# Optimization experiments

Measured on AMD Instinct MI355X. Metric: run time of the kernel, lower is better.

The kernel has to match this reference:

```python
import jax, jax.numpy as jnp
import numpy as np

B = 32          # batch
IH = IW = 32    # image_size
N = IH * IW     # tokens = 1024
INP = 256
OUP = 256
H = 8           # heads
D = 32          # dim_head
INNER = H * D   # 256
TABLE = (2 * IH - 1) * (2 * IW - 1)  # 3969


def _rel_index():
    # exact replica of the torch buffer construction
    coords = np.stack(np.meshgrid(np.arange(IH), np.arange(IW), indexing='ij')).reshape(2, -1)
    rel = coords[:, :, None] - coords[:, None, :]
    rel[0] += IH - 1
    rel[1] += IW - 1
    rel[0] *= 2 * IW - 1
    return (rel[0] + rel[1]).reshape(-1)  # [N*N]


def setup_inputs() -> dict:
    key = jax.random.key(0)
    k0, k1, k2, k3 = jax.random.split(key, 4)
    x = jax.random.normal(k0, (B, N, INP), jnp.float32)
    W_qkv = jax.random.normal(k1, (INP, 3 * INNER), jnp.float32) * 0.02
    bias_table = jax.random.normal(k2, (TABLE, H), jnp.float32) * 0.02
    W_out = jax.random.normal(k3, (INNER, OUP), jnp.float32) * 0.02
    b_out = jnp.zeros((OUP,), jnp.float32)
    rel_index = jnp.asarray(_rel_index(), jnp.int32)
    return {"x": x, "W_qkv": W_qkv, "bias_table": bias_table,
            "W_out": W_out, "b_out": b_out, "rel_index": rel_index}


def reference(x, W_qkv, bias_table, W_out, b_out, rel_index):
    scale = D ** -0.5
    qkv = x @ W_qkv                                   # [B, N, 3*INNER]
    q, k, v = jnp.split(qkv, 3, axis=-1)
    to_heads = lambda t: t.reshape(B, N, H, D).transpose(0, 2, 1, 3)  # b h n d
    q, k, v = to_heads(q), to_heads(k), to_heads(v)
    dots = jnp.einsum('bhid,bhjd->bhij', q, k) * scale  # [B, H, N, N]
    # gather per-head relative position bias: [N*N, H] -> [1, H, N, N]
    bias = bias_table[rel_index].reshape(N, N, H).transpose(2, 0, 1)[None]
    attn = jax.nn.softmax(dots + bias, axis=-1)
    out = jnp.einsum('bhij,bhjd->bhid', attn, v)        # [B, H, N, D]
    out = out.transpose(0, 2, 1, 3).reshape(B, N, INNER)
    return out @ W_out + b_out
```

## Files before the change

kernel.cpp:

```cpp
#include <hip/hip_runtime.h>

typedef __attribute__((ext_vector_type(4))) int            vi4;
typedef __attribute__((ext_vector_type(4))) float          vf4;
typedef __attribute__((ext_vector_type(8))) short          vs8;
typedef __attribute__((ext_vector_type(2))) unsigned int   vu2;
typedef unsigned short u16;
typedef unsigned int   u32;

#define LOG2E  1.4426950408889634f
#define QSCALE 0.2550484109f

static __device__ __forceinline__ u16 f2bf(float f) {
  u32 u = __builtin_bit_cast(u32, f);
  u32 r = (u + 0x7fffu + ((u >> 16) & 1u)) >> 16;
  return (u16)r;
}
static __device__ __forceinline__ float bfu_lo(u32 u) {
  return __builtin_bit_cast(float, u << 16);
}
static __device__ __forceinline__ float bfu_hi(u32 u) {
  return __builtin_bit_cast(float, u & 0xffff0000u);
}
static __device__ __forceinline__ u32 packbf_perm(float a, float b) {
  return __builtin_amdgcn_perm(__builtin_bit_cast(u32, b),
                               __builtin_bit_cast(u32, a), 0x07060302u);
}
static __device__ __forceinline__ vf4 unpack_bias(const u32* grp, int tj) {
  u32 b0 = grp[tj * 2], b1 = grp[tj * 2 + 1];
  vf4 c; c[0] = bfu_lo(b0); c[1] = bfu_hi(b0);
  c[2] = bfu_lo(b1); c[3] = bfu_hi(b1);
  return c;
}

static __device__ __forceinline__ void ldsdma16(void* lds, const void* g) {
  __builtin_amdgcn_global_load_lds(
      (const u32 __attribute__((address_space(1)))*)g,
      (u32 __attribute__((address_space(3)))*)lds, 16, 0, 0);
}

__global__ void prep_all(const float* __restrict__ x, u16* __restrict__ xbf,
                         const float* __restrict__ Wqkv, u16* __restrict__ WqkvT,
                         const float* __restrict__ Wout, u16* __restrict__ WoutT,
                         const int* __restrict__ rel, const float* __restrict__ table,
                         u32* __restrict__ bias_pk, float* __restrict__ bias_f,
                         int use_f32) {
  __shared__ __align__(8) u16 relS[64 * 32];
  int bid = blockIdx.x, tid = threadIdx.x;
  if (bid < 8192) {
    int i = (bid * 256 + tid) * 4;
    vf4 v = *(const vf4*)&x[i];
    u32 lo = (u32)f2bf(v[0]) | ((u32)f2bf(v[1]) << 16);
    u32 hi = (u32)f2bf(v[2]) | ((u32)f2bf(v[3]) << 16);
    vu2 o; o[0] = lo; o[1] = hi;
    *(vu2*)&xbf[i] = o;
  } else if (bid < 9216) {
    const float* src; u16* dst; int C, idx;
    if (bid < 8960) { src = Wqkv; dst = WqkvT; C = 768; idx = (bid - 8192) * 256 + tid; }
    else            { src = Wout; dst = WoutT; C = 256; idx = (bid - 8960) * 256 + tid; }
    int r = idx / C, c = idx - r * C;
    dst[c * 256 + r] = f2bf(src[idx]);
  } else {
    int b2 = bid - 9216;
    int qt = b2 >> 6, t = (b2 >> 2) & 15, s = b2 & 3;
    int ti = s >> 1, jhalf = s & 1;
    int wave = tid >> 6, quad = (tid >> 4) & 3, l15 = tid & 15;
    int jbase = t * 64 + jhalf * 32;

#pragma unroll
    for (int p = 0; p < 2; ++p) {
      int task = p * 256 + tid;
      int q = task >> 3, unit = task & 7;
      int m = qt * 128 + (q >> 4) * 32 + ti * 16 + (q & 15);
      vi4 v = *(const vi4*)&rel[m * 1024 + jbase + unit * 4];
      vu2 pk;
      pk[0] = (u32)(v[0] & 0xffff) | ((u32)v[1] << 16);
      pk[1] = (u32)(v[2] & 0xffff) | ((u32)v[3] << 16);
      *(vu2*)&relS[q * 32 + unit * 4] = pk;
    }
    __syncthreads();

    int mrow = wave * 16 + l15;
    float vals[8][8];
#pragma unroll
    for (int tjl = 0; tjl < 2; ++tjl)
#pragma unroll
      for (int r = 0; r < 4; ++r) {
        int idx = relS[mrow * 32 + tjl * 16 + quad * 4 + r];
        vf4 a = *(const vf4*)&table[idx * 8];
        vf4 bb = *(const vf4*)&table[idx * 8 + 4];
#pragma unroll
        for (int h = 0; h < 4; ++h) {
          vals[tjl * 4 + r][h] = a[h];
          vals[tjl * 4 + r][h + 4] = bb[h];
        }
      }
    if (use_f32) {
#pragma unroll
      for (int h = 0; h < 8; ++h)
#pragma unroll
        for (int tjl = 0; tjl < 2; ++tjl) {
          int frag = ti * 4 + jhalf * 2 + tjl;
          vf4 v;
#pragma unroll
          for (int r = 0; r < 4; ++r) v[r] = vals[tjl * 4 + r][h] * LOG2E;
          *(vf4*)&bias_f[(((h * 8 + qt) * 16 + t) * 8 + frag) * 1024 + tid * 4] = v;
        }
    } else {
#pragma unroll
      for (int h = 0; h < 8; ++h) {
        u32 o[4];
#pragma unroll
        for (int tjl = 0; tjl < 2; ++tjl)
#pragma unroll
          for (int p = 0; p < 2; ++p) {
            u32 lo = f2bf(vals[tjl * 4 + 2 * p][h] * LOG2E);
            u32 hi = f2bf(vals[tjl * 4 + 2 * p + 1][h] * LOG2E);
            o[tjl * 2 + p] = lo | (hi << 16);
          }
        *(vi4*)&bias_pk[h * 524288 + (qt * 16 + t) * 4096 + tid * 16 + s * 4] =
            *(const vi4*)o;
      }
    }
  }
}

template <int EPI>
__global__ __launch_bounds__(256, 2) void gemm_k256(
    const u16* __restrict__ A, const u16* __restrict__ Bt,
    u16* __restrict__ q_out, u16* __restrict__ k_out, u16* __restrict__ v_out,
    float* __restrict__ c_out, const float* __restrict__ bias) {
  __shared__ __align__(16) u16 SMEM[EPI == 0 ? 128 * 136 : 8192];
  u16* As = SMEM;
  u16* Bs = SMEM + 4096;
  const int tid = threadIdx.x;
  const int lane15 = tid & 15, quad = (tid >> 4) & 3, wave = tid >> 6;
  const int wr = (wave & 1) * 64, wc = (wave >> 1) * 64;
  const int m0 = blockIdx.y * 128, n0 = blockIdx.x * 128;

  const u16* Ag = &A[(m0 + (tid >> 2)) * 256 + (tid & 3) * 8];
  const u16* Bg = &Bt[(n0 + (tid >> 2)) * 256 + (tid & 3) * 8];
  u16* AsW = &As[wave * 512];
  u16* BsW = &Bs[wave * 512];

  const vf4 z4 = {0.f, 0.f, 0.f, 0.f};
  vf4 acc[4][4];
#pragma unroll
  for (int i = 0; i < 4; ++i)
#pragma unroll
    for (int j = 0; j < 4; ++j) acc[i][j] = z4;

  for (int k0 = 0; k0 < 256; k0 += 32) {
    __syncthreads();
    ldsdma16(AsW,        Ag + k0);
    ldsdma16(AsW + 2048, Ag + k0 + 64 * 256);
    ldsdma16(BsW,        Bg + k0);
    ldsdma16(BsW + 2048, Bg + k0 + 64 * 256);
    __syncthreads();
    vs8 af[4], bfr[4];
#pragma unroll
    for (int ti = 0; ti < 4; ++ti)
      af[ti] = *(const vs8*)&As[(wr + ti * 16 + lane15) * 32 + quad * 8];
#pragma unroll
    for (int tj = 0; tj < 4; ++tj)
      bfr[tj] = *(const vs8*)&Bs[(wc + tj * 16 + lane15) * 32 + quad * 8];
#pragma unroll
    for (int ti = 0; ti < 4; ++ti)
#pragma unroll
      for (int tj = 0; tj < 4; ++tj)
        acc[ti][tj] = __builtin_amdgcn_mfma_f32_16x16x32_bf16(af[ti], bfr[tj],
                                                              acc[ti][tj], 0, 0, 0);
  }

  if (EPI == 0) {
    const int which = n0 >> 8;
    const int bb = m0 >> 10, nn0 = m0 & 1023;
    u16* Cs = SMEM;
    __syncthreads();
    if (which < 2) {
      float sc = (which == 0) ? QSCALE : 1.f;
#pragma unroll
      for (int tj = 0; tj < 4; ++tj) {
        int col = wc + tj * 16 + lane15;
#pragma unroll
        for (int ti = 0; ti < 4; ++ti) {
          int row0 = wr + ti * 16 + quad * 4;
#pragma unroll
          for (int r = 0; r < 4; ++r)
            Cs[(row0 + r) * 136 + col] = f2bf(acc[ti][tj][r] * sc);
        }
      }
      __syncthreads();
      u16* base = (which == 0) ? q_out : k_out;
#pragma unroll
      for (int hp = 0; hp < 4; ++hp) {
        int hh = ((n0 + hp * 32) >> 5) & 7;
        u16* pb = base + ((bb * 8 + hh) * 1024 + nn0) * 32;
#pragma unroll
        for (int p2 = 0; p2 < 2; ++p2) {
          int task = p2 * 256 + tid;
          int row = task >> 2, unit = task & 3;
          vi4 v = *(const vi4*)&Cs[row * 136 + hp * 32 + unit * 8];
          *(vi4*)&pb[row * 32 + unit * 8] = v;
        }
      }
    } else {
#pragma unroll
      for (int tj = 0; tj < 4; ++tj) {
        int col = wc + tj * 16 + lane15;
#pragma unroll
        for (int ti = 0; ti < 4; ++ti) {
          int row0 = wr + ti * 16 + quad * 4;
          vu2 pk;
          pk[0] = (u32)f2bf(acc[ti][tj][0]) | ((u32)f2bf(acc[ti][tj][1]) << 16);
          pk[1] = (u32)f2bf(acc[ti][tj][2]) | ((u32)f2bf(acc[ti][tj][3]) << 16);
          *(vu2*)&Cs[col * 136 + row0] = pk;
        }
      }
      __syncthreads();
#pragma unroll
      for (int p = 0; p < 8; ++p) {
        int task = p * 256 + tid;
        int col = task >> 4, unit = task & 15;
        int cg = n0 + col;
        int hh = (cg >> 5) & 7, d = cg & 31;
        vi4 v = *(const vi4*)&Cs[col * 136 + unit * 8];
        *(vi4*)&v_out[((bb * 8 + hh) * 32 + d) * 1024 + nn0 + unit * 8] = v;
      }
    }
  } else {
#pragma unroll
    for (int tj = 0; tj < 4; ++tj) {
      int colg = n0 + wc + tj * 16 + lane15;
      float bo = bias[colg];
#pragma unroll
      for (int ti = 0; ti < 4; ++ti)
#pragma unroll
        for (int r = 0; r < 4; ++r) {
          int rowg = m0 + wr + ti * 16 + quad * 4 + r;
          c_out[rowg * 256 + colg] = acc[ti][tj][r] + bo;
        }
    }
  }
}

template <int BF32>
__global__ __launch_bounds__(256, 4) void flash_attn(
    const u16* __restrict__ Qws, const u16* __restrict__ Kws,
    const u16* __restrict__ Vtws, const void* __restrict__ biasv,
    u16* __restrict__ Ows) {
  __shared__ __align__(16) u16 Ks[2][64 * 40];
  __shared__ __align__(16) u16 Vt[2][32 * 72];
  __shared__ __align__(16) u16 Ps[4][32 * 72];

  const int tid = threadIdx.x;
  const int l15 = tid & 15, quad = (tid >> 4) & 3, wave = tid >> 6;
  const int bid = blockIdx.x;
  const int h = bid & 7, b = (bid >> 3) & 31, qt = bid >> 8;
  const int q0 = qt * 128;
  const int bh = b * 8 + h;
  const u16* Qbase = Qws + (bh * 1024 + q0) * 32;
  const u16* Kbase = Kws + bh * 1024 * 32;
  const u16* Vbase = Vtws + bh * 32 * 1024;
  const float* Bf = (const float*)biasv + (h * 8 + qt) * 131072 + tid * 4;
  const u32*  Bpk = (const u32*)biasv + h * 524288 + qt * 65536 + tid * 16;

  const int kv_j = tid >> 2, kv_seg = (tid & 3) * 8;
  const int v_d = tid >> 3,  v_seg = (tid & 7) * 8;
  const u16* Kg = Kbase + kv_j * 32 + kv_seg;
  const u16* Vg = Vbase + v_d * 1024 + v_seg;

  vs8 af[2];
#pragma unroll
  for (int ti = 0; ti < 2; ++ti)
    af[ti] = *(const vs8*)&Qbase[(wave * 32 + ti * 16 + l15) * 32 + quad * 8];

  vi4 kreg = *(const vi4*)Kg;
  vi4 vreg = *(const vi4*)Vg;
  *(vi4*)&Ks[0][kv_j * 40 + kv_seg] = kreg;
  *(vi4*)&Vt[0][v_d * 72 + v_seg] = vreg;

  vf4 b0pre[4];
  vi4 bpk_pre[2];
  if (BF32) {
#pragma unroll
    for (int i = 0; i < 4; ++i) b0pre[i] = *(const vf4*)&Bf[i * 1024];
  } else {
#pragma unroll
    for (int i = 0; i < 2; ++i) bpk_pre[i] = *(const vi4*)(Bpk + i * 4);
  }

  const vf4 z4 = {0.f, 0.f, 0.f, 0.f};
  vf4 O[2][2];
  O[0][0] = z4; O[0][1] = z4; O[1][0] = z4; O[1][1] = z4;
  vf4 Lacc[2];
  Lacc[0] = z4; Lacc[1] = z4;

  vs8 onesv;
#pragma unroll
  for (int i = 0; i < 8; ++i) onesv[i] = (short)0x3F80;

  u16* PwBase = Ps[wave];

  for (int t = 0; t < 16; ++t) {
    const int cur = t & 1, nxt = cur ^ 1;
    __syncthreads();

    if (t < 15) {
      kreg = *(const vi4*)(Kg + (t + 1) * 2048);
      vreg = *(const vi4*)(Vg + (t + 1) * 64);
    }
    vf4 b1cur[4], b0nxt[4];
    vi4 bpk1[2], bpk_n[2];
    if (BF32) {
#pragma unroll
      for (int i = 0; i < 4; ++i)
        b1cur[i] = *(const vf4*)&Bf[(t * 8 + 4 + i) * 1024];
      if (t < 15) {
#pragma unroll
        for (int i = 0; i < 4; ++i)
          b0nxt[i] = *(const vf4*)&Bf[((t + 1) * 8 + i) * 1024];
      }
    } else {
      bpk1[0] = *(const vi4*)(Bpk + t * 4096 + 8);
      bpk1[1] = *(const vi4*)(Bpk + t * 4096 + 12);
      if (t < 15) {
        bpk_n[0] = *(const vi4*)(Bpk + (t + 1) * 4096);
        bpk_n[1] = *(const vi4*)(Bpk + (t + 1) * 4096 + 4);
      }
    }

    vs8 bk[4];
#pragma unroll
    for (int tj = 0; tj < 4; ++tj)
      bk[tj] = *(const vs8*)&Ks[cur][(tj * 16 + l15) * 40 + quad * 8];

#pragma unroll
    for (int tj = 0; tj < 4; ++tj) {
      vf4 c = BF32 ? b0pre[tj] : unpack_bias((const u32*)bpk_pre, tj);
      vf4 st = __builtin_amdgcn_mfma_f32_16x16x32_bf16(bk[tj], af[0], c, 0, 0, 0);
      float p0 = __builtin_exp2f(st[0]);
      float p1 = __builtin_exp2f(st[1]);
      float p2 = __builtin_exp2f(st[2]);
      float p3 = __builtin_exp2f(st[3]);
      vu2 pk; pk[0] = packbf_perm(p0, p1); pk[1] = packbf_perm(p2, p3);
      *(vu2*)&PwBase[l15 * 72 + tj * 16 + quad * 4] = pk;
    }
#pragma unroll
    for (int tj = 0; tj < 4; ++tj) {
      vf4 c = BF32 ? b1cur[tj] : unpack_bias((const u32*)bpk1, tj);
      vf4 st = __builtin_amdgcn_mfma_f32_16x16x32_bf16(bk[tj], af[1], c, 0, 0, 0);
      float p0 = __builtin_exp2f(st[0]);
      float p1 = __builtin_exp2f(st[1]);
      float p2 = __builtin_exp2f(st[2]);
      float p3 = __builtin_exp2f(st[3]);
      vu2 pk; pk[0] = packbf_perm(p0, p1); pk[1] = packbf_perm(p2, p3);
      *(vu2*)&PwBase[(16 + l15) * 72 + tj * 16 + quad * 4] = pk;
    }

#pragma unroll
    for (int kk = 0; kk < 2; ++kk) {
      vs8 pf[2], bv[2];
#pragma unroll
      for (int ti = 0; ti < 2; ++ti)
        pf[ti] = *(const vs8*)&PwBase[(ti * 16 + l15) * 72 + kk * 32 + quad * 8];
#pragma unroll
      for (int tj2 = 0; tj2 < 2; ++tj2)
        bv[tj2] = *(const vs8*)&Vt[cur][(tj2 * 16 + l15) * 72 + kk * 32 + quad * 8];
#pragma unroll
      for (int ti = 0; ti < 2; ++ti) {
#pragma unroll
        for (int tj2 = 0; tj2 < 2; ++tj2)
          O[ti][tj2] = __builtin_amdgcn_mfma_f32_16x16x32_bf16(bv[tj2], pf[ti],
                                                               O[ti][tj2], 0, 0, 0);
        Lacc[ti] = __builtin_amdgcn_mfma_f32_16x16x32_bf16(onesv, pf[ti],
                                                           Lacc[ti], 0, 0, 0);
      }
    }

    if (t < 15) {
      *(vi4*)&Ks[nxt][kv_j * 40 + kv_seg] = kreg;
      *(vi4*)&Vt[nxt][v_d * 72 + v_seg] = vreg;
      if (BF32) {
#pragma unroll
        for (int i = 0; i < 4; ++i) b0pre[i] = b0nxt[i];
      } else {
        bpk_pre[0] = bpk_n[0]; bpk_pre[1] = bpk_n[1];
      }
    }
  }

#pragma unroll
  for (int ti = 0; ti < 2; ++ti) {
    float inv = __builtin_amdgcn_rcpf(Lacc[ti][0]);
    int m = q0 + wave * 32 + ti * 16 + l15;
    int rowbase = (b * 1024 + m) * 256 + h * 32;
#pragma unroll
    for (int tj2 = 0; tj2 < 2; ++tj2) {
      u32 lo = (u32)f2bf(O[ti][tj2][0] * inv) | ((u32)f2bf(O[ti][tj2][1] * inv) << 16);
      u32 hi = (u32)f2bf(O[ti][tj2][2] * inv) | ((u32)f2bf(O[ti][tj2][3] * inv) << 16);
      vu2 pk; pk[0] = lo; pk[1] = hi;
      *(vu2*)&Ows[rowbase + tj2 * 16 + quad * 4] = pk;
    }
  }
}

extern "C" void kernel_launch(void* const* d_in, const int* in_sizes, int n_in,
                              void* d_out, int out_size, void* d_ws, size_t ws_size,
                              hipStream_t stream) {
  (void)in_sizes; (void)n_in; (void)out_size;
  const float* x     = (const float*)d_in[0];
  const float* Wqkv  = (const float*)d_in[1];
  const float* table = (const float*)d_in[2];
  const float* Wout  = (const float*)d_in[3];
  const float* bout  = (const float*)d_in[4];
  const int*   rel   = (const int*)d_in[5];
  float* out = (float*)d_out;

  const int use_f32 = (ws_size >= 101187584ull) ? 1 : 0;
  const size_t bias_bytes = use_f32 ? 33554432ull : 16777216ull;

  char* ws = (char*)d_ws;
  u16* xbf    = (u16*)(ws);
  u16* Qws    = (u16*)(ws + 16777216);
  u16* Kws    = (u16*)(ws + 33554432);
  u16* Vtws   = (u16*)(ws + 50331648);
  void* biasp = (void*)(ws + 67108864);
  u16* WqkvT  = (u16*)(ws + 67108864 + bias_bytes);
  u16* WoutT  = WqkvT + 196608;

  prep_all<<<9728, 256, 0, stream>>>(x, xbf, Wqkv, WqkvT, Wout, WoutT,
                                     rel, table, (u32*)biasp, (float*)biasp,
                                     use_f32);
  gemm_k256<0><<<dim3(6, 256), 256, 0, stream>>>(xbf, WqkvT, Qws, Kws, Vtws,
                                                 nullptr, nullptr);
  if (use_f32)
    flash_attn<1><<<2048, 256, 0, stream>>>(Qws, Kws, Vtws, biasp, xbf);
  else
    flash_attn<0><<<2048, 256, 0, stream>>>(Qws, Kws, Vtws, biasp, xbf);
  gemm_k256<1><<<dim3(2, 256), 256, 0, stream>>>(xbf, WoutT,
                                                 nullptr, nullptr, nullptr, out, bout);
}
```

Before: 225.5 us.

## Keep softmax P in registers and feed PV via 16x16x16 MFMA

Removes the per-wave LDS staging buffer for the probability tile. The QK^T MFMA output layout is reused directly as the B operand of 16x16x16 bf16 MFMAs for PV and the row-sum, which drops LDS writes and reads and a shared-memory allocation. It also raises wave priority around the compute block and moves next-tile bias loads to the end of the iteration. The cost is twice as many smaller MFMAs for PV, and the bias prefetch now has less time to hide its latency.

```diff
diff --git a/kernel.cpp b/kernel.cpp
--- a/kernel.cpp
+++ b/kernel.cpp
@@ -3,6 +3,7 @@
 typedef __attribute__((ext_vector_type(4))) int            vi4;
 typedef __attribute__((ext_vector_type(4))) float          vf4;
 typedef __attribute__((ext_vector_type(8))) short          vs8;
+typedef __attribute__((ext_vector_type(4))) short          vs4;
 typedef __attribute__((ext_vector_type(2))) unsigned int   vu2;
 typedef unsigned short u16;
 typedef unsigned int   u32;
@@ -250,7 +251,6 @@
     u16* __restrict__ Ows) {
   __shared__ __align__(16) u16 Ks[2][64 * 40];
   __shared__ __align__(16) u16 Vt[2][32 * 72];
-  __shared__ __align__(16) u16 Ps[4][32 * 72];
 
   const int tid = threadIdx.x;
   const int l15 = tid & 15, quad = (tid >> 4) & 3, wave = tid >> 6;
@@ -295,11 +295,12 @@
   vf4 Lacc[2];
   Lacc[0] = z4; Lacc[1] = z4;
 
-  vs8 onesv;
-#pragma unroll
-  for (int i = 0; i < 8; ++i) onesv[i] = (short)0x3F80;
-
-  u16* PwBase = Ps[wave];
+  vs4 ones4;
+#pragma unroll
+  for (int i = 0; i < 4; ++i) ones4[i] = (short)0x3F80;
+
+  const int ks_off = l15 * 40 + quad * 8;
+  const int vt_off = l15 * 72 + quad * 4;
 
   for (int t = 0; t < 16; ++t) {
     const int cur = t & 1, nxt = cur ^ 1;
@@ -309,82 +310,51 @@
       kreg = *(const vi4*)(Kg + (t + 1) * 2048);
       vreg = *(const vi4*)(Vg + (t + 1) * 64);
     }
-    vf4 b1cur[4], b0nxt[4];
-    vi4 bpk1[2], bpk_n[2];
+    vf4 b1cur[4];
+    vi4 bpk1[2];
     if (BF32) {
 #pragma unroll
       for (int i = 0; i < 4; ++i)
         b1cur[i] = *(const vf4*)&Bf[(t * 8 + 4 + i) * 1024];
-      if (t < 15) {
-#pragma unroll
-        for (int i = 0; i < 4; ++i)
-          b0nxt[i] = *(const vf4*)&Bf[((t + 1) * 8 + i) * 1024];
-      }
     } else {
       bpk1[0] = *(const vi4*)(Bpk + t * 4096 + 8);
       bpk1[1] = *(const vi4*)(Bpk + t * 4096 + 12);
-      if (t < 15) {
-        bpk_n[0] = *(const vi4*)(Bpk + (t + 1) * 4096);
-        bpk_n[1] = *(const vi4*)(Bpk + (t + 1) * 4096 + 4);
-      }
-    }
-
-    vs8 bk[4];
-#pragma unroll
-    for (int tj = 0; tj < 4; ++tj)
-      bk[tj] = *(const vs8*)&Ks[cur][(tj * 16 + l15) * 40 + quad * 8];
-
+    }
+
+    __builtin_amdgcn_s_setprio(1);
 #pragma unroll
     for (int tj = 0; tj < 4; ++tj) {
-      vf4 c = BF32 ? b0pre[tj] : unpack_bias((const u32*)bpk_pre, tj);
-      vf4 st = __builtin_amdgcn_mfma_f32_16x16x32_bf16(bk[tj], af[0], c, 0, 0, 0);
-      float p0 = __builtin_exp2f(st[0]);
-      float p1 = __builtin_exp2f(st[1]);
-      float p2 = __builtin_exp2f(st[2]);
-      float p3 = __builtin_exp2f(st[3]);
-      vu2 pk; pk[0] = packbf_perm(p0, p1); pk[1] = packbf_perm(p2, p3);
-      *(vu2*)&PwBase[l15 * 72 + tj * 16 + quad * 4] = pk;
-    }
-#pragma unroll
-    for (int tj = 0; tj < 4; ++tj) {
-      vf4 c = BF32 ? b1cur[tj] : unpack_bias((const u32*)bpk1, tj);
-      vf4 st = __builtin_amdgcn_mfma_f32_16x16x32_bf16(bk[tj], af[1], c, 0, 0, 0);
-      float p0 = __builtin_exp2f(st[0]);
-      float p1 = __builtin_exp2f(st[1]);
-      float p2 = __builtin_exp2f(st[2]);
-      float p3 = __builtin_exp2f(st[3]);
-      vu2 pk; pk[0] = packbf_perm(p0, p1); pk[1] = packbf_perm(p2, p3);
-      *(vu2*)&PwBase[(16 + l15) * 72 + tj * 16 + quad * 4] = pk;
-    }
-
-#pragma unroll
-    for (int kk = 0; kk < 2; ++kk) {
-      vs8 pf[2], bv[2];
-#pragma unroll
-      for (int ti = 0; ti < 2; ++ti)
-        pf[ti] = *(const vs8*)&PwBase[(ti * 16 + l15) * 72 + kk * 32 + quad * 8];
-#pragma unroll
-      for (int tj2 = 0; tj2 < 2; ++tj2)
-        bv[tj2] = *(const vs8*)&Vt[cur][(tj2 * 16 + l15) * 72 + kk * 32 + quad * 8];
+      vs8 bk = *(const vs8*)&Ks[cur][tj * 640 + ks_off];
+      vs4 va0 = *(const vs4*)&Vt[cur][vt_off + tj * 16];
+      vs4 va1 = *(const vs4*)&Vt[cur][vt_off + 1152 + tj * 16];
 #pragma unroll
       for (int ti = 0; ti < 2; ++ti) {
-#pragma unroll
-        for (int tj2 = 0; tj2 < 2; ++tj2)
-          O[ti][tj2] = __builtin_amdgcn_mfma_f32_16x16x32_bf16(bv[tj2], pf[ti],
-                                                               O[ti][tj2], 0, 0, 0);
-        Lacc[ti] = __builtin_amdgcn_mfma_f32_16x16x32_bf16(onesv, pf[ti],
-                                                           Lacc[ti], 0, 0, 0);
-      }
-    }
+        vf4 c = BF32 ? (ti ? b1cur[tj] : b0pre[tj])
+                     : unpack_bias((const u32*)(ti ? bpk1 : bpk_pre), tj);
+        vf4 st = __builtin_amdgcn_mfma_f32_16x16x32_bf16(bk, af[ti], c, 0, 0, 0);
+        float p0 = __builtin_exp2f(st[0]);
+        float p1 = __builtin_exp2f(st[1]);
+        float p2 = __builtin_exp2f(st[2]);
+        float p3 = __builtin_exp2f(st[3]);
+        vu2 pw; pw[0] = packbf_perm(p0, p1); pw[1] = packbf_perm(p2, p3);
+        vs4 pf = __builtin_bit_cast(vs4, pw);
+        O[ti][0] = __builtin_amdgcn_mfma_f32_16x16x16bf16_1k(va0, pf, O[ti][0], 0, 0, 0);
+        O[ti][1] = __builtin_amdgcn_mfma_f32_16x16x16bf16_1k(va1, pf, O[ti][1], 0, 0, 0);
+        Lacc[ti] = __builtin_amdgcn_mfma_f32_16x16x16bf16_1k(ones4, pf, Lacc[ti], 0, 0, 0);
+      }
+    }
+    __builtin_amdgcn_s_setprio(0);
 
     if (t < 15) {
       *(vi4*)&Ks[nxt][kv_j * 40 + kv_seg] = kreg;
       *(vi4*)&Vt[nxt][v_d * 72 + v_seg] = vreg;
       if (BF32) {
 #pragma unroll
-        for (int i = 0; i < 4; ++i) b0pre[i] = b0nxt[i];
+        for (int i = 0; i < 4; ++i)
+          b0pre[i] = *(const vf4*)&Bf[((t + 1) * 8 + i) * 1024];
       } else {
-        bpk_pre[0] = bpk_n[0]; bpk_pre[1] = bpk_n[1];
+        bpk_pre[0] = *(const vi4*)(Bpk + (t + 1) * 4096);
+        bpk_pre[1] = *(const vi4*)(Bpk + (t + 1) * 4096 + 4);
       }
     }
   }
```

Result: no change. 226.4 us (+0.4%).
